# Kernel tuning notes

Measured on AMD Instinct MI355X. Metric: run time of the kernel, lower is better.

The kernel has to match this reference:

```python
import jax, jax.numpy as jnp
import numpy as np

B, N, D = 4, 2048, 768
H, HD = 12, 64  # heads, head_dim; D == H*HD
SCALE = HD ** -0.5


def setup_inputs() -> dict:
    key = jax.random.key(0)
    k1, k2, k3 = jax.random.split(key, 3)
    x = jax.random.normal(k1, (B, N, D), dtype=jnp.float32)
    w_qkv = jax.random.normal(k2, (D, 3 * D), dtype=jnp.float32) * (D ** -0.5)
    b_qkv = jnp.zeros((3 * D,), dtype=jnp.float32)
    w_proj = jax.random.normal(k3, (D, D), dtype=jnp.float32) * (D ** -0.5)
    b_proj = jnp.zeros((D,), dtype=jnp.float32)
    return {"x": x, "w_qkv": w_qkv, "b_qkv": b_qkv, "w_proj": w_proj, "b_proj": b_proj}


def reference(x, w_qkv, b_qkv, w_proj, b_proj):
    # 1. QKV projection, split into 3
    qkv = x @ w_qkv + b_qkv                      # (B, N, 3D)
    q, k, v = jnp.split(qkv, 3, axis=-1)         # each (B, N, D)
    # 2. reshape to (B, H, N, HD)
    def to_heads(t):
        return t.reshape(B, N, H, HD).transpose(0, 2, 1, 3)
    q, k, v = to_heads(q), to_heads(k), to_heads(v)
    # 3-4. scaled dot-product attention (full score matrix, as in the original)
    scores = jnp.einsum("bhnd,bhmd->bhnm", q, k) * SCALE   # (B, H, N, N)
    attn = jax.nn.softmax(scores, axis=-1)
    # 5. dropout p=0.0 -> identity (eval)
    # 6. weighted sum
    out = jnp.einsum("bhnm,bhmd->bhnd", attn, v)           # (B, H, N, HD)
    # 7. merge heads
    out = out.transpose(0, 2, 1, 3).reshape(B, N, D)
    # 8. output projection
    return out @ w_proj + b_proj
```

## Files before the change

kernel.cpp:

```cpp
#include <hip/hip_runtime.h>
#include <stdint.h>
#include <stddef.h>


typedef __bf16 bf16x8 __attribute__((ext_vector_type(8)));
typedef float  f32x4  __attribute__((ext_vector_type(4)));
typedef float  f32x16 __attribute__((ext_vector_type(16)));
typedef unsigned int u32x2 __attribute__((ext_vector_type(2)));

__device__ __forceinline__ float bf2f(unsigned short u){
  union { unsigned int i; float f; } x; x.i = ((unsigned int)u) << 16; return x.f;
}
__device__ __forceinline__ unsigned short fast2bf(float f){
  union { float f; unsigned int i; } x; x.f = f;
  return (unsigned short)((x.i + 0x8000u) >> 16);
}
__device__ __forceinline__ unsigned int fbits(float f){
  union { float f; unsigned int i; } x; x.f = f; return x.i;
}
__device__ __forceinline__ unsigned int cvtpk_bf16(float lo, float hi){
  unsigned int r;
  asm("v_cvt_pk_bf16_f32 %0, %1, %2" : "=v"(r) : "v"(lo), "v"(hi));
  return r;
}
__device__ __forceinline__ void plswap32(unsigned int &a, unsigned int &b){
#if __has_builtin(__builtin_amdgcn_permlane32_swap)
  u32x2 r = __builtin_amdgcn_permlane32_swap(a, b, false, false);
  a = r.x; b = r.y;
#else
  asm volatile("v_permlane32_swap_b32 %0, %1" : "+v"(a), "+v"(b));
#endif
}

#if __has_builtin(__builtin_amdgcn_exp2f)
  #define EXP2F(x) __builtin_amdgcn_exp2f(x)
#else
  #define EXP2F(x) exp2f(x)
#endif

#define GLD16(gp, lp) __builtin_amdgcn_global_load_lds( \
  (__attribute__((address_space(1))) void*)(uintptr_t)(gp), \
  (__attribute__((address_space(3))) void*)(unsigned int)(uintptr_t)(lp), 16, 0, 0)

__global__ void f32_to_bf16(const float* __restrict__ in,
                            unsigned short* __restrict__ out, int n){
  int i = (blockIdx.x * 256 + threadIdx.x) * 4;
  if(i < n){
    float4 v = *(const float4*)(in + i);
    ushort4 o;
    o.x = fast2bf(v.x); o.y = fast2bf(v.y); o.z = fast2bf(v.z); o.w = fast2bf(v.w);
    *(ushort4*)(out + i) = o;
  }
}

__global__ void transpose_f32_bf16(const float* __restrict__ W,
                                   unsigned short* __restrict__ Wt, int K, int N){
  __shared__ float tile[32][33];
  int n0 = blockIdx.x * 32, k0 = blockIdx.y * 32;
  int tx = threadIdx.x, ty = threadIdx.y;
  for(int i = ty; i < 32; i += 8) tile[i][tx] = W[(size_t)(k0 + i) * N + (n0 + tx)];
  __syncthreads();
  for(int i = ty; i < 32; i += 8) Wt[(size_t)(n0 + i) * K + (k0 + tx)] = fast2bf(tile[tx][i]);
}

__global__ __launch_bounds__(256) void transpose_v(const unsigned short* __restrict__ qkv,
                                                   unsigned short* __restrict__ VT){
  __shared__ __align__(16) unsigned short Ts[64*72];
  const int t  = threadIdx.x;
  const int jt = blockIdx.x;
  const int bh = blockIdx.y;
  const int b = bh / 12, h = bh - b*12;
  const unsigned short* src = qkv + (size_t)(b*2048 + jt*64)*2304 + 1536 + h*64;
  #pragma unroll
  for(int c = t; c < 512; c += 256){
    int j = c >> 3, d0 = (c & 7) * 8;
    *(uint4*)&Ts[j*72 + d0] = *(const uint4*)(src + (size_t)j*2304 + d0);
  }
  __syncthreads();
  unsigned short* dst = VT + (size_t)bh*64*2048 + jt*64;
  #pragma unroll
  for(int c = t; c < 512; c += 256){
    int d = c >> 3, j0 = (c & 7) * 8;
    ushort4 lo, hi;
    lo.x = Ts[(j0+0)*72 + d]; lo.y = Ts[(j0+1)*72 + d];
    lo.z = Ts[(j0+2)*72 + d]; lo.w = Ts[(j0+3)*72 + d];
    hi.x = Ts[(j0+4)*72 + d]; hi.y = Ts[(j0+5)*72 + d];
    hi.z = Ts[(j0+6)*72 + d]; hi.w = Ts[(j0+7)*72 + d];
    *(ushort4*)(dst + (size_t)d*2048 + j0)     = lo;
    *(ushort4*)(dst + (size_t)d*2048 + j0 + 4) = hi;
  }
}

template<typename OT>
__global__ __launch_bounds__(256) void gemm_bt(const unsigned short* __restrict__ A,
                                               const unsigned short* __restrict__ Bt,
                                               const float* __restrict__ bias,
                                               OT* __restrict__ C,
                                               int M, int N, int K, int lda){
  __shared__ __align__(16) unsigned short As[2][128*32];
  __shared__ __align__(16) unsigned short Bs[2][128*32];
  const int tid  = threadIdx.x;
  const int lane = tid & 63, w = tid >> 6;
  const int m0 = blockIdx.y * 128, n0 = blockIdx.x * 128;

  f32x4 acc[4][4];
  #pragma unroll
  for(int i=0;i<4;i++)
    #pragma unroll
    for(int j=0;j<4;j++) acc[i][j] = (f32x4){0.f,0.f,0.f,0.f};

  const int c0 = w*64 + lane, c1 = c0 + 256;
  const unsigned short* Ag0 = A  + (size_t)(m0 + (c0>>2)) * lda + (c0&3)*8;
  const unsigned short* Ag1 = A  + (size_t)(m0 + (c1>>2)) * lda + (c1&3)*8;
  const unsigned short* Bg0 = Bt + (size_t)(n0 + (c0>>2)) * K   + (c0&3)*8;
  const unsigned short* Bg1 = Bt + (size_t)(n0 + (c1>>2)) * K   + (c1&3)*8;

  const int wm = w & 1, wn = w >> 1;
  const int quad = lane >> 4, l15 = lane & 15;

  GLD16(Ag0, As[0] +        w*512);
  GLD16(Ag1, As[0] + 2048 + w*512);
  GLD16(Bg0, Bs[0] +        w*512);
  GLD16(Bg1, Bs[0] + 2048 + w*512);

  int cur = 0;
  for(int kt = 0; kt < K; kt += 32){
    __syncthreads();
    if(kt + 32 < K){
      int nx = cur ^ 1;
      GLD16(Ag0 + kt + 32, As[nx] +        w*512);
      GLD16(Ag1 + kt + 32, As[nx] + 2048 + w*512);
      GLD16(Bg0 + kt + 32, Bs[nx] +        w*512);
      GLD16(Bg1 + kt + 32, Bs[nx] + 2048 + w*512);
    }

    bf16x8 af[4], bfr[4];
    #pragma unroll
    for(int mt=0;mt<4;mt++) af[mt]  = *(const bf16x8*)&As[cur][(wm*64 + mt*16 + l15)*32 + quad*8];
    #pragma unroll
    for(int nt=0;nt<4;nt++) bfr[nt] = *(const bf16x8*)&Bs[cur][(wn*64 + nt*16 + l15)*32 + quad*8];
    #pragma unroll
    for(int mt=0;mt<4;mt++)
      #pragma unroll
      for(int nt=0;nt<4;nt++)
        acc[mt][nt] = __builtin_amdgcn_mfma_f32_16x16x32_bf16(af[mt], bfr[nt], acc[mt][nt], 0, 0, 0);
    cur ^= 1;
  }

  #pragma unroll
  for(int nt=0;nt<4;nt++){
    int col = n0 + wn*64 + nt*16 + l15;
    float bv = bias[col];
    #pragma unroll
    for(int mt=0;mt<4;mt++){
      int row0 = m0 + wm*64 + mt*16 + quad*4;
      #pragma unroll
      for(int i=0;i<4;i++){
        float v = acc[mt][nt][i] + bv;
        if constexpr (sizeof(OT) == 2)
          C[(size_t)(row0 + i) * N + col] = (OT)fast2bf(v);
        else
          C[(size_t)(row0 + i) * N + col] = (OT)v;
      }
    }
  }
}

__global__ __launch_bounds__(256, 3) void attn_mfma(unsigned short* __restrict__ qkv,
                                                    const unsigned short* __restrict__ VT){
  __shared__ __align__(16) unsigned short Ks[2][64*64];
  __shared__ __align__(16) unsigned short Vs[2][64*64];
  __shared__ float linv_lds[4*32];

  const int t    = threadIdx.x;
  const int lane = t & 63, w = t >> 6;
  const int l31  = lane & 31, hi = lane >> 5;
  const int sx   = l31 & 7;

  const int bid = blockIdx.x;
  const int wg  = (bid & 7) * 96 + (bid >> 3);
  const int b   = wg / 192;
  const int rem = wg - b * 192;
  const int h   = rem >> 4;
  const int bx  = rem & 15;
  const int q0  = bx * 128 + w * 32;

  unsigned short* Qg = qkv + (size_t)(b*2048 + q0)*2304 + h*64;

  const float QSCALE = 0.125f * 1.4426950408889634f;
  bf16x8 qf[4];
  #pragma unroll
  for(int c=0;c<4;c++){
    uint4 raw = *(const uint4*)(Qg + (size_t)l31*2304 + c*16 + hi*8);
    const unsigned short* rp = (const unsigned short*)&raw;
    unsigned short o[8];
    #pragma unroll
    for(int e=0;e<8;e++) o[e] = fast2bf(bf2f(rp[e]) * QSCALE);
    qf[c] = *(const bf16x8*)o;
  }

  f32x16 oacc0, oacc1;
  #pragma unroll
  for(int i=0;i<16;i++){ oacc0[i] = 0.f; oacc1[i] = 0.f; }
  float lpart = 0.f;

  const int r8 = lane >> 3, c8 = lane & 7;
  const int scw = c8 ^ r8;
  const unsigned short* gK = qkv + (size_t)(b*2048)*2304 + 768 + h*64;
  const unsigned short* gV = VT + (size_t)(b*12 + h)*64*2048;
  const size_t kOffA = (size_t)(w*8 + r8)*2304 + scw*8;
  const size_t kOffB = kOffA + (size_t)32*2304;
  const size_t vOffA = (size_t)(w*8 + r8)*2048 + scw*8;
  const size_t vOffB = vOffA + (size_t)32*2048;

  GLD16(gK + kOffA, Ks[0] +        w*512);
  GLD16(gK + kOffB, Ks[0] + 2048 + w*512);
  GLD16(gV + vOffA, Vs[0] +        w*512);
  GLD16(gV + vOffB, Vs[0] + 2048 + w*512);

  int cur = 0;
  #pragma unroll 1
  for(int it = 0; it < 32; ++it){
    __syncthreads();
    if(it + 1 < 32){
      int nx = cur ^ 1;
      gK += (size_t)64*2304;
      gV += 64;
      GLD16(gK + kOffA, Ks[nx] +        w*512);
      GLD16(gK + kOffB, Ks[nx] + 2048 + w*512);
      GLD16(gV + vOffA, Vs[nx] +        w*512);
      GLD16(gV + vOffB, Vs[nx] + 2048 + w*512);
    }
    const unsigned short* Kst = Ks[cur];
    const unsigned short* Vst = Vs[cur];

    #pragma unroll
    for(int ks = 0; ks < 2; ++ks){
      bf16x8 kf[4];
      #pragma unroll
      for(int c=0;c<4;c++)
        kf[c] = *(const bf16x8*)&Kst[(ks*32 + l31)*64 + (((c*2 + hi) ^ sx) * 8)];

      f32x16 sacc;
      #pragma unroll
      for(int i=0;i<16;i++) sacc[i] = 0.f;
      sacc = __builtin_amdgcn_mfma_f32_32x32x16_bf16(kf[0], qf[0], sacc, 0, 0, 0);
      sacc = __builtin_amdgcn_mfma_f32_32x32x16_bf16(kf[1], qf[1], sacc, 0, 0, 0);
      sacc = __builtin_amdgcn_mfma_f32_32x32x16_bf16(kf[2], qf[2], sacc, 0, 0, 0);
      sacc = __builtin_amdgcn_mfma_f32_32x32x16_bf16(kf[3], qf[3], sacc, 0, 0, 0);

      bf16x8 vf00 = *(const bf16x8*)&Vst[(     l31)*64 + (((ks*4 + 0 + hi) ^ sx) * 8)];
      bf16x8 vf01 = *(const bf16x8*)&Vst[(32 + l31)*64 + (((ks*4 + 0 + hi) ^ sx) * 8)];
      bf16x8 vf10 = *(const bf16x8*)&Vst[(     l31)*64 + (((ks*4 + 2 + hi) ^ sx) * 8)];
      bf16x8 vf11 = *(const bf16x8*)&Vst[(32 + l31)*64 + (((ks*4 + 2 + hi) ^ sx) * 8)];

      float p[16];
      #pragma unroll
      for(int r=0;r<16;r++){ p[r] = EXP2F(sacc[r]); lpart += p[r]; }

      unsigned int d0 = cvtpk_bf16(p[0],  p[1]);
      unsigned int d1 = cvtpk_bf16(p[2],  p[3]);
      unsigned int d2 = cvtpk_bf16(p[4],  p[5]);
      unsigned int d3 = cvtpk_bf16(p[6],  p[7]);
      unsigned int d4 = cvtpk_bf16(p[8],  p[9]);
      unsigned int d5 = cvtpk_bf16(p[10], p[11]);
      unsigned int d6 = cvtpk_bf16(p[12], p[13]);
      unsigned int d7 = cvtpk_bf16(p[14], p[15]);
      plswap32(d0, d2); plswap32(d1, d3);
      plswap32(d4, d6); plswap32(d5, d7);
      unsigned int c0w[4] = {d0, d1, d2, d3};
      unsigned int c1w[4] = {d4, d5, d6, d7};
      bf16x8 pa0 = *(const bf16x8*)c0w;
      bf16x8 pa1 = *(const bf16x8*)c1w;

      oacc0 = __builtin_amdgcn_mfma_f32_32x32x16_bf16(pa0, vf00, oacc0, 0, 0, 0);
      oacc1 = __builtin_amdgcn_mfma_f32_32x32x16_bf16(pa0, vf01, oacc1, 0, 0, 0);
      oacc0 = __builtin_amdgcn_mfma_f32_32x32x16_bf16(pa1, vf10, oacc0, 0, 0, 0);
      oacc1 = __builtin_amdgcn_mfma_f32_32x32x16_bf16(pa1, vf11, oacc1, 0, 0, 0);
    }
    cur ^= 1;
  }

  lpart += __shfl_xor(lpart, 32, 64);
  if(lane < 32) linv_lds[w*32 + l31] = 1.0f / lpart;
  __syncthreads();

  #pragma unroll
  for(int r=0;r<16;r++){
    int qrow = (r&3) + 8*(r>>2) + 4*hi;
    float li = linv_lds[w*32 + qrow];
    unsigned short* row = Qg + (size_t)qrow*2304;
    row[l31]      = fast2bf(oacc0[r] * li);
    row[32 + l31] = fast2bf(oacc1[r] * li);
  }
}

extern "C" void kernel_launch(void* const* d_in, const int* in_sizes, int n_in,
                              void* d_out, int out_size, void* d_ws, size_t ws_size,
                              hipStream_t stream){
  const float* x      = (const float*)d_in[0];
  const float* w_qkv  = (const float*)d_in[1];
  const float* b_qkv  = (const float*)d_in[2];
  const float* w_proj = (const float*)d_in[3];
  const float* b_proj = (const float*)d_in[4];
  float* out = (float*)d_out;

  unsigned short* xb      = (unsigned short*)d_ws;
  unsigned short* Wt_qkv  = xb      + (size_t)8192*768;
  unsigned short* Wt_proj = Wt_qkv  + (size_t)2304*768;
  unsigned short* qkvb    = Wt_proj + (size_t)768*768;
  unsigned short* VT      = xb;

  f32_to_bf16<<<(8192*768)/1024, 256, 0, stream>>>(x, xb, 8192*768);
  transpose_f32_bf16<<<dim3(72, 24), dim3(32, 8), 0, stream>>>(w_qkv,  Wt_qkv,  768, 2304);
  transpose_f32_bf16<<<dim3(24, 24), dim3(32, 8), 0, stream>>>(w_proj, Wt_proj, 768, 768);

  gemm_bt<unsigned short><<<dim3(2304/128, 8192/128), 256, 0, stream>>>(
      xb, Wt_qkv, b_qkv, qkvb, 8192, 2304, 768, 768);

  transpose_v<<<dim3(32, 48), 256, 0, stream>>>(qkvb, VT);

  attn_mfma<<<768, 256, 0, stream>>>(qkvb, VT);

  gemm_bt<float><<<dim3(768/128, 8192/128), 256, 0, stream>>>(
      qkvb, Wt_proj, b_proj, out, 8192, 768, 768, 2304);
}
```

Baseline: 217.5 us.

## Store K/V tiles in LDS in MFMA fragment order, add setprio and split sums

Result: no change. 220.6 us (+1.5%).

```diff
diff --git a/kernel.cpp b/kernel.cpp
--- a/kernel.cpp
+++ b/kernel.cpp
@@ -168,14 +168,13 @@
 
 __global__ __launch_bounds__(256, 3) void attn_mfma(unsigned short* __restrict__ qkv,
                                                     const unsigned short* __restrict__ VT){
-  __shared__ __align__(16) unsigned short Ks[2][64*64];
-  __shared__ __align__(16) unsigned short Vs[2][64*64];
+  __shared__ __align__(16) unsigned short Ks[2][4096];
+  __shared__ __align__(16) unsigned short Vs[2][4096];
   __shared__ float linv_lds[4*32];
 
   const int t    = threadIdx.x;
   const int lane = t & 63, w = t >> 6;
   const int l31  = lane & 31, hi = lane >> 5;
-  const int sx   = l31 & 7;
 
   const int bid = blockIdx.x;
   const int wg  = (bid & 7) * 96 + (bid >> 3);
@@ -202,21 +201,20 @@
   f32x16 oacc0, oacc1;
   #pragma unroll
   for(int i=0;i<16;i++){ oacc0[i] = 0.f; oacc1[i] = 0.f; }
-  float lpart = 0.f;
-
-  const int r8 = lane >> 3, c8 = lane & 7;
-  const int scw = c8 ^ r8;
+  float lp0=0.f, lp1=0.f, lp2=0.f, lp3=0.f;
+
+  const int gA = w*2, gB = w*2 + 1;
   const unsigned short* gK = qkv + (size_t)(b*2048)*2304 + 768 + h*64;
   const unsigned short* gV = VT + (size_t)(b*12 + h)*64*2048;
-  const size_t kOffA = (size_t)(w*8 + r8)*2304 + scw*8;
-  const size_t kOffB = kOffA + (size_t)32*2304;
-  const size_t vOffA = (size_t)(w*8 + r8)*2048 + scw*8;
-  const size_t vOffB = vOffA + (size_t)32*2048;
-
-  GLD16(gK + kOffA, Ks[0] +        w*512);
-  GLD16(gK + kOffB, Ks[0] + 2048 + w*512);
-  GLD16(gV + vOffA, Vs[0] +        w*512);
-  GLD16(gV + vOffB, Vs[0] + 2048 + w*512);
+  const size_t kOffA = (size_t)((gA>>2)*32 + l31)*2304 + (gA&3)*16 + hi*8;
+  const size_t kOffB = (size_t)((gB>>2)*32 + l31)*2304 + (gB&3)*16 + hi*8;
+  const size_t vOffA = (size_t)((gA&1)*32 + l31)*2048 + (gA>>2)*32 + ((gA>>1)&1)*16 + hi*8;
+  const size_t vOffB = (size_t)((gB&1)*32 + l31)*2048 + (gB>>2)*32 + ((gB>>1)&1)*16 + hi*8;
+
+  GLD16(gK + kOffA, Ks[0] + gA*512);
+  GLD16(gK + kOffB, Ks[0] + gB*512);
+  GLD16(gV + vOffA, Vs[0] + gA*512);
+  GLD16(gV + vOffB, Vs[0] + gB*512);
 
   int cur = 0;
   #pragma unroll 1
@@ -226,37 +224,43 @@
       int nx = cur ^ 1;
       gK += (size_t)64*2304;
       gV += 64;
-      GLD16(gK + kOffA, Ks[nx] +        w*512);
-      GLD16(gK + kOffB, Ks[nx] + 2048 + w*512);
-      GLD16(gV + vOffA, Vs[nx] +        w*512);
-      GLD16(gV + vOffB, Vs[nx] + 2048 + w*512);
+      GLD16(gK + kOffA, Ks[nx] + gA*512);
+      GLD16(gK + kOffB, Ks[nx] + gB*512);
+      GLD16(gV + vOffA, Vs[nx] + gA*512);
+      GLD16(gV + vOffB, Vs[nx] + gB*512);
     }
-    const unsigned short* Kst = Ks[cur];
-    const unsigned short* Vst = Vs[cur];
+    const unsigned short* Kst = Ks[cur] + lane*8;
+    const unsigned short* Vst = Vs[cur] + lane*8;
 
     #pragma unroll
     for(int ks = 0; ks < 2; ++ks){
-      bf16x8 kf[4];
-      #pragma unroll
-      for(int c=0;c<4;c++)
-        kf[c] = *(const bf16x8*)&Kst[(ks*32 + l31)*64 + (((c*2 + hi) ^ sx) * 8)];
+      bf16x8 kf0 = *(const bf16x8*)(Kst + (ks*4 + 0)*512);
+      bf16x8 kf1 = *(const bf16x8*)(Kst + (ks*4 + 1)*512);
+      bf16x8 kf2 = *(const bf16x8*)(Kst + (ks*4 + 2)*512);
+      bf16x8 kf3 = *(const bf16x8*)(Kst + (ks*4 + 3)*512);
 
       f32x16 sacc;
       #pragma unroll
       for(int i=0;i<16;i++) sacc[i] = 0.f;
-      sacc = __builtin_amdgcn_mfma_f32_32x32x16_bf16(kf[0], qf[0], sacc, 0, 0, 0);
-      sacc = __builtin_amdgcn_mfma_f32_32x32x16_bf16(kf[1], qf[1], sacc, 0, 0, 0);
-      sacc = __builtin_amdgcn_mfma_f32_32x32x16_bf16(kf[2], qf[2], sacc, 0, 0, 0);
-      sacc = __builtin_amdgcn_mfma_f32_32x32x16_bf16(kf[3], qf[3], sacc, 0, 0, 0);
-
-      bf16x8 vf00 = *(const bf16x8*)&Vst[(     l31)*64 + (((ks*4 + 0 + hi) ^ sx) * 8)];
-      bf16x8 vf01 = *(const bf16x8*)&Vst[(32 + l31)*64 + (((ks*4 + 0 + hi) ^ sx) * 8)];
-      bf16x8 vf10 = *(const bf16x8*)&Vst[(     l31)*64 + (((ks*4 + 2 + hi) ^ sx) * 8)];
-      bf16x8 vf11 = *(const bf16x8*)&Vst[(32 + l31)*64 + (((ks*4 + 2 + hi) ^ sx) * 8)];
+      __builtin_amdgcn_s_setprio(1);
+      sacc = __builtin_amdgcn_mfma_f32_32x32x16_bf16(kf0, qf[0], sacc, 0, 0, 0);
+      sacc = __builtin_amdgcn_mfma_f32_32x32x16_bf16(kf1, qf[1], sacc, 0, 0, 0);
+      sacc = __builtin_amdgcn_mfma_f32_32x32x16_bf16(kf2, qf[2], sacc, 0, 0, 0);
+      sacc = __builtin_amdgcn_mfma_f32_32x32x16_bf16(kf3, qf[3], sacc, 0, 0, 0);
+      __builtin_amdgcn_s_setprio(0);
+
+      bf16x8 vf00 = *(const bf16x8*)(Vst + (ks*4 + 0)*512);
+      bf16x8 vf01 = *(const bf16x8*)(Vst + (ks*4 + 1)*512);
+      bf16x8 vf10 = *(const bf16x8*)(Vst + (ks*4 + 2)*512);
+      bf16x8 vf11 = *(const bf16x8*)(Vst + (ks*4 + 3)*512);
 
       float p[16];
       #pragma unroll
-      for(int r=0;r<16;r++){ p[r] = EXP2F(sacc[r]); lpart += p[r]; }
+      for(int r=0;r<16;r++) p[r] = EXP2F(sacc[r]);
+      #pragma unroll
+      for(int r=0;r<16;r+=4){
+        lp0 += p[r]; lp1 += p[r+1]; lp2 += p[r+2]; lp3 += p[r+3];
+      }
 
       unsigned int d0 = cvtpk_bf16(p[0],  p[1]);
       unsigned int d1 = cvtpk_bf16(p[2],  p[3]);
@@ -273,14 +277,17 @@
       bf16x8 pa0 = *(const bf16x8*)c0w;
       bf16x8 pa1 = *(const bf16x8*)c1w;
 
+      __builtin_amdgcn_s_setprio(1);
       oacc0 = __builtin_amdgcn_mfma_f32_32x32x16_bf16(pa0, vf00, oacc0, 0, 0, 0);
       oacc1 = __builtin_amdgcn_mfma_f32_32x32x16_bf16(pa0, vf01, oacc1, 0, 0, 0);
       oacc0 = __builtin_amdgcn_mfma_f32_32x32x16_bf16(pa1, vf10, oacc0, 0, 0, 0);
       oacc1 = __builtin_amdgcn_mfma_f32_32x32x16_bf16(pa1, vf11, oacc1, 0, 0, 0);
+      __builtin_amdgcn_s_setprio(0);
     }
     cur ^= 1;
   }
 
+  float lpart = (lp0 + lp1) + (lp2 + lp3);
   lpart += __shfl_xor(lpart, 32, 64);
   if(lane < 32) linv_lds[w*32 + l31] = 1.0f / lpart;
   __syncthreads();
```
